# Optimization experiments

Measured on AMD Instinct MI355X. Metric: run time of the kernel, lower is better.

The kernel has to match this reference:

```python
import jax, jax.numpy as jnp
import numpy as np
from jax import lax

K = 32          # num_units (ring size / channels)
T = 100         # num_iters
FAR, NEAR = 29, 9
RING_MIN, RING_MAX, RING_BW = -0.5, 0.1, 0.5
NEAR_SUM = FAR_SUM = 0.4
H_STEP, TAU, DECAY_K = 1.0, 5.0, 1.0   # step_size, time_constant, decay_constant


def _ring_weight():
    # FeatureConnections._kernel: min-max-scaled gaussian bump, rolled per out-channel.
    X = np.linspace(0.0, 1.0, K)
    base = np.exp(-0.5 * ((X - X[K // 2]) / RING_BW) ** 2)  # pdf normalization cancels in min-max
    base = (base - base.min()) / (base.max() - base.min())
    base = base * (RING_MAX - RING_MIN) + RING_MIN
    W = np.stack([np.roll(base, K // 2 + i) for i in range(K)])  # (K_out, K_in)
    return W.astype(np.float32)


def _surround_kernel():
    # SpatialConnections._kernel: near excitation, far inhibition (opponent surround).
    inh = -FAR_SUM / (FAR ** 2 - NEAR ** 2)
    exc = NEAR_SUM / NEAR ** 2
    k = np.full((FAR, FAR), inh, dtype=np.float32)
    u = FAR // 2 - NEAR // 2
    v = FAR // 2 + NEAR // 2 + 1
    k[u:v, u:v] = exc
    return k


def setup_inputs() -> dict:
    key = jax.random.key(0)
    k1, k2, k3 = jax.random.split(key, 3)
    inbound = jax.random.normal(k1, (2, K, 64, 64), dtype=jnp.float32)
    Wf = jnp.asarray(_ring_weight())                                   # (K, K) 1x1 channel mixing
    bf = jax.random.normal(k2, (K,), dtype=jnp.float32) * 0.01        # Conv2d bias (random init in source)
    Ws = jnp.asarray(np.broadcast_to(_surround_kernel(), (K, FAR, FAR)).copy())  # diagonal (depthwise) taps
    bs = jax.random.normal(k3, (K,), dtype=jnp.float32) * 0.01
    return {"inbound": inbound, "Wf": Wf, "bf": bf, "Ws": Ws, "bs": bs}


def reference(inbound, Wf, bf, Ws, bs):
    decay = 1.0 - H_STEP * DECAY_K ** 2 / TAU   # 0.8
    gain = H_STEP / TAU                          # 0.2
    dw = Ws[:, None]                             # (K, 1, FAR, FAR) depthwise kernel (diag of full KxK conv)

    def feat(X):  # 1x1 ring-attractor channel mix
        return jnp.einsum('oi,nihw->nohw', Wf, X) + bf[None, :, None, None]

    def spat(X):  # depthwise opponent-surround conv, 'SAME' == padding (FAR-1)//2
        y = lax.conv_general_dilated(X, dw, (1, 1), 'SAME',
                                     dimension_numbers=('NCHW', 'OIHW', 'NCHW'),
                                     feature_group_count=K)
        return y + bs[None, :, None, None]

    drive = 0.5 * inbound

    def step(X, _):
        S = drive + feat(X) + spat(X)
        Xn = decay * X + gain * jax.nn.relu(S)
        return Xn, Xn

    X0 = jnp.zeros_like(inbound)
    _, Xt = lax.scan(step, X0, None, length=T)   # (T, N, K, H, W)
    return jnp.transpose(Xt, (1, 0, 2, 3, 4))    # (N, T, K, H, W)
```

## Files before the change

kernel.cpp:

```cpp
#include <hip/hip_runtime.h>

#define NN 2
#define KC 32
#define TT 100
#define HH 64
#define WW 64
#define HWSZ (HH*WW)
#define RB 4
#define RROWS 16
#define HALO 14
#define BROWS (RROWS + 2*HALO)
#define SW 65
#define NWG (NN*KC*RB)
#define FLAG_STRIDE 16

typedef float fx4 __attribute__((ext_vector_type(4)));

#define GLD8(x0,x1,x2,x3,x4,x5,x6,x7,p0,p1,p2,p3,p4,p5,p6,p7) \
  asm volatile( \
    "global_load_dwordx4 %0, %8, off sc0 sc1\n\t" \
    "global_load_dwordx4 %1, %9, off sc0 sc1\n\t" \
    "global_load_dwordx4 %2, %10, off sc0 sc1\n\t" \
    "global_load_dwordx4 %3, %11, off sc0 sc1\n\t" \
    "global_load_dwordx4 %4, %12, off sc0 sc1\n\t" \
    "global_load_dwordx4 %5, %13, off sc0 sc1\n\t" \
    "global_load_dwordx4 %6, %14, off sc0 sc1\n\t" \
    "global_load_dwordx4 %7, %15, off sc0 sc1" \
    : "=&v"(x0),"=&v"(x1),"=&v"(x2),"=&v"(x3), \
      "=&v"(x4),"=&v"(x5),"=&v"(x6),"=&v"(x7) \
    : "v"(p0),"v"(p1),"v"(p2),"v"(p3),"v"(p4),"v"(p5),"v"(p6),"v"(p7) \
    : "memory")

#define GLD3(x0,x1,x2,p0,p1,p2) \
  asm volatile( \
    "global_load_dwordx4 %0, %3, off sc0 sc1\n\t" \
    "global_load_dwordx4 %1, %4, off sc0 sc1\n\t" \
    "global_load_dwordx4 %2, %5, off sc0 sc1" \
    : "=&v"(x0),"=&v"(x1),"=&v"(x2) \
    : "v"(p0),"v"(p1),"v"(p2) : "memory")

#define VWAIT8(x0,x1,x2,x3,x4,x5,x6,x7) \
  asm volatile("s_waitcnt vmcnt(0)" \
    : "+v"(x0),"+v"(x1),"+v"(x2),"+v"(x3),"+v"(x4),"+v"(x5),"+v"(x6),"+v"(x7) \
    :: "memory")
#define VWAIT3(x0,x1,x2) \
  asm volatile("s_waitcnt vmcnt(0)" : "+v"(x0),"+v"(x1),"+v"(x2) :: "memory")

#define GST4(p, v) \
  asm volatile("global_store_dwordx4 %0, %1, off sc0 sc1" :: "v"(p), "v"(v) : "memory")

#define BAR_LDS()  asm volatile("s_waitcnt lgkmcnt(0)\n\ts_barrier" ::: "memory")
#define BAR_ONLY() asm volatile("s_barrier" ::: "memory")
#define BAR_FULL() asm volatile("s_waitcnt vmcnt(0) lgkmcnt(0)\n\ts_barrier" ::: "memory")

#define ACC(V, ch) do { const float w_ = wf[(ch)]; \
    s0 += w_*(V)[0]; s1 += w_*(V)[1]; s2 += w_*(V)[2]; s3 += w_*(V)[3]; \
    if ((ch) == c) xold = (V); } while (0)

__device__ __forceinline__ float wave_incl_scan(float v, int lane) {
  #pragma unroll
  for (int d = 1; d < 64; d <<= 1) {
    float o = __shfl_up(v, (unsigned)d, 64);
    if (lane >= d) v += o;
  }
  return v;
}

__global__ void __launch_bounds__(256, 1) ring_kernel(
    const float* __restrict__ inbound, const float* __restrict__ Wf,
    const float* __restrict__ bf, const float* __restrict__ Ws,
    const float* __restrict__ bs, float* __restrict__ out,
    unsigned* __restrict__ flags)
{
  __shared__ float I[BROWS*SW];

  const int b    = blockIdx.x;
  const int n    = b >> 7;
  const int c    = (b >> 2) & (KC-1);
  const int rb   = b & (RB-1);
  const int tid  = threadIdx.x;
  const int lane = tid & 63;
  const int wave = tid >> 6;
  const int r0   = rb * RROWS;

  const float inh = Ws[0];
  const float exc = Ws[14*29 + 14];
  const float w9  = exc - inh;

  float wf[KC];
  #pragma unroll
  for (int i = 0; i < KC; ++i) wf[i] = Wf[c*KC + i];
  const float bsum = bf[c] + bs[c];

  const int off = rb*(RROWS*WW) + tid*4;
  const float* drp = inbound + (size_t)(n*KC + c)*HWSZ + off;
  const float base0 = 0.5f*drp[0] + bsum;
  const float base1 = 0.5f*drp[1] + bsum;
  const float base2 = 0.5f*drp[2] + bsum;
  const float base3 = 0.5f*drp[3] + bsum;

  const int rl = tid >> 4;
  const int w0 = (tid & 15) * 4;
  const int br = rl + HALO;

  int  hlofs[3], hgofs[3];
  bool hval[3];
  #pragma unroll
  for (int q = 0; q < 3; ++q) {
    int id  = tid + q*256; if (id > 703) id = 703;
    int row = id >> 4;
    int c4  = (id & 15) * 4;
    int g   = r0 - HALO + row;
    hval[q]  = (g >= 0 && g < HH);
    int gc   = g < 0 ? 0 : (g > HH-1 ? HH-1 : g);
    hgofs[q] = gc*WW + c4;
    hlofs[q] = row*SW + c4;
  }

  const int ownf = ((n<<7) | (c<<2) | rb) * FLAG_STRIDE;
  int pollf = ownf;
  if (tid < 32)                  pollf = ((n<<7) | (tid<<2) | rb)    * FLAG_STRIDE;
  else if (tid == 32 && rb>0)    pollf = ((n<<7) | (c<<2) | (rb-1))  * FLAG_STRIDE;
  else if (tid == 33 && rb<RB-1) pollf = ((n<<7) | (c<<2) | (rb+1))  * FLAG_STRIDE;
  unsigned* pollp = flags + pollf;
  unsigned* ownp  = flags + ownf;

  for (int t = 0; t < TT; ++t) {
    const float* Xprev = out + (size_t)((n*TT + (t-1))*KC)*HWSZ;

    fx4 A0,A1,A2v,A3v,A4,A5,A6,A7;
    fx4 B0,B1,B2,B3,B4,B5,B6,B7;
    fx4 h0,h1,h2;

    if (t > 0) {
      if (tid < 34) {
        const unsigned tgt = (unsigned)t;
        while (__hip_atomic_load(pollp, __ATOMIC_RELAXED, __HIP_MEMORY_SCOPE_AGENT) < tgt) {
          __builtin_amdgcn_s_sleep(1);
        }
      }
      BAR_ONLY();

      const float* Xc = Xprev + (size_t)c*HWSZ;
      GLD3(h0,h1,h2, (const fx4*)(Xc+hgofs[0]),
                     (const fx4*)(Xc+hgofs[1]),
                     (const fx4*)(Xc+hgofs[2]));
      const float* Xp = Xprev + off;
      GLD8(A0,A1,A2v,A3v,A4,A5,A6,A7,
           (const fx4*)(Xp+(size_t)0*HWSZ),(const fx4*)(Xp+(size_t)1*HWSZ),
           (const fx4*)(Xp+(size_t)2*HWSZ),(const fx4*)(Xp+(size_t)3*HWSZ),
           (const fx4*)(Xp+(size_t)4*HWSZ),(const fx4*)(Xp+(size_t)5*HWSZ),
           (const fx4*)(Xp+(size_t)6*HWSZ),(const fx4*)(Xp+(size_t)7*HWSZ));
      GLD8(B0,B1,B2,B3,B4,B5,B6,B7,
           (const fx4*)(Xp+(size_t)8*HWSZ),(const fx4*)(Xp+(size_t)9*HWSZ),
           (const fx4*)(Xp+(size_t)10*HWSZ),(const fx4*)(Xp+(size_t)11*HWSZ),
           (const fx4*)(Xp+(size_t)12*HWSZ),(const fx4*)(Xp+(size_t)13*HWSZ),
           (const fx4*)(Xp+(size_t)14*HWSZ),(const fx4*)(Xp+(size_t)15*HWSZ));

      VWAIT3(h0,h1,h2);
      if (!hval[0]) h0 = fx4{0.f,0.f,0.f,0.f};
      if (!hval[1]) h1 = fx4{0.f,0.f,0.f,0.f};
      if (!hval[2]) h2 = fx4{0.f,0.f,0.f,0.f};
      I[hlofs[0]+0]=h0[0]; I[hlofs[0]+1]=h0[1]; I[hlofs[0]+2]=h0[2]; I[hlofs[0]+3]=h0[3];
      I[hlofs[1]+0]=h1[0]; I[hlofs[1]+1]=h1[1]; I[hlofs[1]+2]=h1[2]; I[hlofs[1]+3]=h1[3];
      I[hlofs[2]+0]=h2[0]; I[hlofs[2]+1]=h2[1]; I[hlofs[2]+2]=h2[2]; I[hlofs[2]+3]=h2[3];
    } else {
      for (int l = tid; l < BROWS*WW; l += 256) I[(l>>6)*SW + (l&63)] = 0.f;
    }
    BAR_LDS();

    #pragma unroll
    for (int k = 0; k < 11; ++k) {
      int row = wave*11 + k;
      float v = I[row*SW + lane];
      v = wave_incl_scan(v, lane);
      I[row*SW + lane] = v;
    }
    BAR_LDS();

    #pragma unroll
    for (int k = 0; k < 16; ++k) {
      int col = wave*16 + k;
      float v = (lane < BROWS) ? I[lane*SW + col] : 0.f;
      v = wave_incl_scan(v, lane);
      if (lane < BROWS) I[lane*SW + col] = v;
    }
    BAR_LDS();

    float s[4];
    #pragma unroll
    for (int j = 0; j < 4; ++j) {
      int w = w0 + j;
      int hi  = br + 14, lo  = br - 15;
      int whi = (w + 14 > 63) ? 63 : (w + 14);
      int wlo = w - 15;
      float b29 = I[hi*SW + whi];
      if (wlo >= 0) b29 -= I[hi*SW + wlo];
      if (lo  >= 0) { b29 -= I[lo*SW + whi]; if (wlo >= 0) b29 += I[lo*SW + wlo]; }
      int hi2  = br + 4, lo2 = br - 5;
      int whi2 = (w + 4 > 63) ? 63 : (w + 4);
      int wlo2 = w - 5;
      float b9 = I[hi2*SW + whi2];
      if (wlo2 >= 0) b9 -= I[hi2*SW + wlo2];
      b9 -= I[lo2*SW + whi2];
      if (wlo2 >= 0) b9 += I[lo2*SW + wlo2];
      s[j] = inh*b29 + w9*b9;
    }
    float s0 = base0 + s[0], s1 = base1 + s[1], s2 = base2 + s[2], s3 = base3 + s[3];

    fx4 xold = fx4{0.f,0.f,0.f,0.f};
    if (t > 0) {
      const float* Xp = Xprev + off;
      VWAIT8(A0,A1,A2v,A3v,A4,A5,A6,A7);
      VWAIT8(B0,B1,B2,B3,B4,B5,B6,B7);
      ACC(A0,0); ACC(A1,1); ACC(A2v,2); ACC(A3v,3);
      ACC(A4,4); ACC(A5,5); ACC(A6,6);  ACC(A7,7);
      GLD8(A0,A1,A2v,A3v,A4,A5,A6,A7,
           (const fx4*)(Xp+(size_t)16*HWSZ),(const fx4*)(Xp+(size_t)17*HWSZ),
           (const fx4*)(Xp+(size_t)18*HWSZ),(const fx4*)(Xp+(size_t)19*HWSZ),
           (const fx4*)(Xp+(size_t)20*HWSZ),(const fx4*)(Xp+(size_t)21*HWSZ),
           (const fx4*)(Xp+(size_t)22*HWSZ),(const fx4*)(Xp+(size_t)23*HWSZ));
      ACC(B0,8);  ACC(B1,9);  ACC(B2,10); ACC(B3,11);
      ACC(B4,12); ACC(B5,13); ACC(B6,14); ACC(B7,15);
      GLD8(B0,B1,B2,B3,B4,B5,B6,B7,
           (const fx4*)(Xp+(size_t)24*HWSZ),(const fx4*)(Xp+(size_t)25*HWSZ),
           (const fx4*)(Xp+(size_t)26*HWSZ),(const fx4*)(Xp+(size_t)27*HWSZ),
           (const fx4*)(Xp+(size_t)28*HWSZ),(const fx4*)(Xp+(size_t)29*HWSZ),
           (const fx4*)(Xp+(size_t)30*HWSZ),(const fx4*)(Xp+(size_t)31*HWSZ));
      VWAIT8(A0,A1,A2v,A3v,A4,A5,A6,A7);
      VWAIT8(B0,B1,B2,B3,B4,B5,B6,B7);
      ACC(A0,16); ACC(A1,17); ACC(A2v,18); ACC(A3v,19);
      ACC(A4,20); ACC(A5,21); ACC(A6,22);  ACC(A7,23);
      ACC(B0,24); ACC(B1,25); ACC(B2,26);  ACC(B3,27);
      ACC(B4,28); ACC(B5,29); ACC(B6,30);  ACC(B7,31);
    }

    fx4 xn;
    xn[0] = 0.8f*xold[0] + 0.2f*fmaxf(s0, 0.f);
    xn[1] = 0.8f*xold[1] + 0.2f*fmaxf(s1, 0.f);
    xn[2] = 0.8f*xold[2] + 0.2f*fmaxf(s2, 0.f);
    xn[3] = 0.8f*xold[3] + 0.2f*fmaxf(s3, 0.f);
    float* po = out + (size_t)((n*TT + t)*KC + c)*HWSZ + off;
    GST4((fx4*)po, xn);

    if (t < TT-1) {
      BAR_FULL();
      if (tid == 0) {
        __hip_atomic_store(ownp, (unsigned)(t+1), __ATOMIC_RELAXED,
                           __HIP_MEMORY_SCOPE_AGENT);
      }
    }
  }
}

extern "C" void kernel_launch(void* const* d_in, const int* in_sizes, int n_in,
                              void* d_out, int out_size, void* d_ws, size_t ws_size,
                              hipStream_t stream) {
  const float* inbound = (const float*)d_in[0];
  const float* Wf      = (const float*)d_in[1];
  const float* bf      = (const float*)d_in[2];
  const float* Ws      = (const float*)d_in[3];
  const float* bs      = (const float*)d_in[4];
  float* out = (float*)d_out;
  unsigned* flags = (unsigned*)d_ws;

  hipMemsetAsync(d_ws, 0, NWG*FLAG_STRIDE*sizeof(unsigned), stream);

  void* args[] = {(void*)&inbound, (void*)&Wf, (void*)&bf, (void*)&Ws,
                  (void*)&bs, (void*)&out, (void*)&flags};
  hipLaunchCooperativeKernel((void*)ring_kernel, dim3(NWG), dim3(256),
                             args, 0, stream);
}
```

Baseline: 1.014 ms.

## Process four channels per workgroup, reusing channel-mix loads and per-wave integral images

Each workgroup now owns a group of four channels instead of one, so the 32-channel loads of the previous state are shared across four outputs and the total grid shrinks from 256 to 64 workgroups. Each wave builds the integral image for one channel using serial per-lane row and column scans instead of shuffle-based wave scans, and the own-channel previous state is kept in registers instead of being picked out of the loaded tiles. The t=0 step skips the zeroed integral-image pass entirely. This cuts redundant global traffic and the number of workgroups that poll flags, but uses fewer CUs and adds serial LDS scan work per wave.

```diff
diff --git a/kernel.cpp b/kernel.cpp
--- a/kernel.cpp
+++ b/kernel.cpp
@@ -2,6 +2,8 @@
 
 #define NN 2
 #define KC 32
+#define G  4
+#define CG (KC/G)
 #define TT 100
 #define HH 64
 #define WW 64
@@ -11,11 +13,14 @@
 #define HALO 14
 #define BROWS (RROWS + 2*HALO)
 #define SW 65
-#define NWG (NN*KC*RB)
+#define TSZ (BROWS*SW)
+#define NWG (NN*CG*RB)
 #define FLAG_STRIDE 16
 
 typedef float fx4 __attribute__((ext_vector_type(4)));
 
+#define GLD1(x, p) \
+  asm volatile("global_load_dwordx4 %0, %1, off sc0 sc1" : "=&v"(x) : "v"(p) : "memory")
 #define GLD8(x0,x1,x2,x3,x4,x5,x6,x7,p0,p1,p2,p3,p4,p5,p6,p7) \
   asm volatile( \
     "global_load_dwordx4 %0, %8, off sc0 sc1\n\t" \
@@ -30,41 +35,20 @@
       "=&v"(x4),"=&v"(x5),"=&v"(x6),"=&v"(x7) \
     : "v"(p0),"v"(p1),"v"(p2),"v"(p3),"v"(p4),"v"(p5),"v"(p6),"v"(p7) \
     : "memory")
-
-#define GLD3(x0,x1,x2,p0,p1,p2) \
-  asm volatile( \
-    "global_load_dwordx4 %0, %3, off sc0 sc1\n\t" \
-    "global_load_dwordx4 %1, %4, off sc0 sc1\n\t" \
-    "global_load_dwordx4 %2, %5, off sc0 sc1" \
-    : "=&v"(x0),"=&v"(x1),"=&v"(x2) \
-    : "v"(p0),"v"(p1),"v"(p2) : "memory")
-
 #define VWAIT8(x0,x1,x2,x3,x4,x5,x6,x7) \
   asm volatile("s_waitcnt vmcnt(0)" \
-    : "+v"(x0),"+v"(x1),"+v"(x2),"+v"(x3),"+v"(x4),"+v"(x5),"+v"(x6),"+v"(x7) \
-    :: "memory")
-#define VWAIT3(x0,x1,x2) \
-  asm volatile("s_waitcnt vmcnt(0)" : "+v"(x0),"+v"(x1),"+v"(x2) :: "memory")
-
+    : "+v"(x0),"+v"(x1),"+v"(x2),"+v"(x3),"+v"(x4),"+v"(x5),"+v"(x6),"+v"(x7) :: "memory")
+#define VWAIT11(x0,x1,x2,x3,x4,x5,x6,x7,x8,x9,x10) \
+  asm volatile("s_waitcnt vmcnt(0)" \
+    : "+v"(x0),"+v"(x1),"+v"(x2),"+v"(x3),"+v"(x4),"+v"(x5), \
+      "+v"(x6),"+v"(x7),"+v"(x8),"+v"(x9),"+v"(x10) :: "memory")
 #define GST4(p, v) \
   asm volatile("global_store_dwordx4 %0, %1, off sc0 sc1" :: "v"(p), "v"(v) : "memory")
 
 #define BAR_LDS()  asm volatile("s_waitcnt lgkmcnt(0)\n\ts_barrier" ::: "memory")
 #define BAR_ONLY() asm volatile("s_barrier" ::: "memory")
 #define BAR_FULL() asm volatile("s_waitcnt vmcnt(0) lgkmcnt(0)\n\ts_barrier" ::: "memory")
-
-#define ACC(V, ch) do { const float w_ = wf[(ch)]; \
-    s0 += w_*(V)[0]; s1 += w_*(V)[1]; s2 += w_*(V)[2]; s3 += w_*(V)[3]; \
-    if ((ch) == c) xold = (V); } while (0)
-
-__device__ __forceinline__ float wave_incl_scan(float v, int lane) {
-  #pragma unroll
-  for (int d = 1; d < 64; d <<= 1) {
-    float o = __shfl_up(v, (unsigned)d, 64);
-    if (lane >= d) v += o;
-  }
-  return v;
-}
+#define LGKM0()    asm volatile("s_waitcnt lgkmcnt(0)" ::: "memory")
 
 __global__ void __launch_bounds__(256, 1) ring_kernel(
     const float* __restrict__ inbound, const float* __restrict__ Wf,
@@ -72,68 +56,80 @@
     const float* __restrict__ bs, float* __restrict__ out,
     unsigned* __restrict__ flags)
 {
-  __shared__ float I[BROWS*SW];
+  __shared__ float T[G*TSZ];
+  __shared__ fx4   WFS[KC];
 
   const int b    = blockIdx.x;
-  const int n    = b >> 7;
-  const int c    = (b >> 2) & (KC-1);
+  const int n    = b >> 5;
+  const int cg   = (b >> 2) & (CG-1);
   const int rb   = b & (RB-1);
   const int tid  = threadIdx.x;
   const int lane = tid & 63;
   const int wave = tid >> 6;
   const int r0   = rb * RROWS;
+  const int ch0  = cg * G;
 
   const float inh = Ws[0];
   const float exc = Ws[14*29 + 14];
   const float w9  = exc - inh;
 
-  float wf[KC];
+  if (tid < KC) {
+    fx4 wv;
+    wv[0] = Wf[(ch0+0)*KC + tid]; wv[1] = Wf[(ch0+1)*KC + tid];
+    wv[2] = Wf[(ch0+2)*KC + tid]; wv[3] = Wf[(ch0+3)*KC + tid];
+    WFS[tid] = wv;
+  }
+  BAR_LDS();
+
+  const int off = r0*WW + tid*4;
+  const int rl  = tid >> 4;
+  const int w0  = (tid & 15) * 4;
+  const int br  = rl + HALO;
+
+  fx4 base[G];
   #pragma unroll
-  for (int i = 0; i < KC; ++i) wf[i] = Wf[c*KC + i];
-  const float bsum = bf[c] + bs[c];
-
-  const int off = rb*(RROWS*WW) + tid*4;
-  const float* drp = inbound + (size_t)(n*KC + c)*HWSZ + off;
-  const float base0 = 0.5f*drp[0] + bsum;
-  const float base1 = 0.5f*drp[1] + bsum;
-  const float base2 = 0.5f*drp[2] + bsum;
-  const float base3 = 0.5f*drp[3] + bsum;
-
-  const int rl = tid >> 4;
-  const int w0 = (tid & 15) * 4;
-  const int br = rl + HALO;
-
-  int  hlofs[3], hgofs[3];
-  bool hval[3];
+  for (int j = 0; j < G; ++j) {
+    const float* dp = inbound + (size_t)(n*KC + ch0 + j)*HWSZ + off;
+    float bsum = bf[ch0+j] + bs[ch0+j];
+    base[j][0] = 0.5f*dp[0] + bsum; base[j][1] = 0.5f*dp[1] + bsum;
+    base[j][2] = 0.5f*dp[2] + bsum; base[j][3] = 0.5f*dp[3] + bsum;
+  }
+
+  int  sgofs[11], slofs[11]; bool sval[11];
   #pragma unroll
-  for (int q = 0; q < 3; ++q) {
-    int id  = tid + q*256; if (id > 703) id = 703;
+  for (int q = 0; q < 11; ++q) {
+    int id  = lane + 64*q;
     int row = id >> 4;
     int c4  = (id & 15) * 4;
     int g   = r0 - HALO + row;
-    hval[q]  = (g >= 0 && g < HH);
+    sval[q]  = (g >= 0 && g < HH);
     int gc   = g < 0 ? 0 : (g > HH-1 ? HH-1 : g);
-    hgofs[q] = gc*WW + c4;
-    hlofs[q] = row*SW + c4;
-  }
-
-  const int ownf = ((n<<7) | (c<<2) | rb) * FLAG_STRIDE;
+    sgofs[q] = gc*WW + c4;
+    slofs[q] = row*SW + c4;
+  }
+  float* Tw = T + wave*TSZ;
+
+  const int ownf = ((n<<5) | (cg<<2) | rb) * FLAG_STRIDE;
   int pollf = ownf;
-  if (tid < 32)                  pollf = ((n<<7) | (tid<<2) | rb)    * FLAG_STRIDE;
-  else if (tid == 32 && rb>0)    pollf = ((n<<7) | (c<<2) | (rb-1))  * FLAG_STRIDE;
-  else if (tid == 33 && rb<RB-1) pollf = ((n<<7) | (c<<2) | (rb+1))  * FLAG_STRIDE;
+  if (tid < CG)                  pollf = ((n<<5) | (tid<<2) | rb)    * FLAG_STRIDE;
+  else if (tid == 8 && rb>0)     pollf = ((n<<5) | (cg<<2) | (rb-1)) * FLAG_STRIDE;
+  else if (tid == 9 && rb<RB-1)  pollf = ((n<<5) | (cg<<2) | (rb+1)) * FLAG_STRIDE;
   unsigned* pollp = flags + pollf;
   unsigned* ownp  = flags + ownf;
 
+  fx4 xn[G];
+  #pragma unroll
+  for (int j = 0; j < G; ++j) xn[j] = fx4{0.f,0.f,0.f,0.f};
+
   for (int t = 0; t < TT; ++t) {
-    const float* Xprev = out + (size_t)((n*TT + (t-1))*KC)*HWSZ;
-
-    fx4 A0,A1,A2v,A3v,A4,A5,A6,A7;
-    fx4 B0,B1,B2,B3,B4,B5,B6,B7;
-    fx4 h0,h1,h2;
+    fx4 sf[G], acc[G];
+    #pragma unroll
+    for (int j = 0; j < G; ++j) { sf[j] = fx4{0,0,0,0}; acc[j] = fx4{0,0,0,0}; }
 
     if (t > 0) {
-      if (tid < 34) {
+      const float* Xprev = out + (size_t)((n*TT + (t-1))*KC)*HWSZ;
+
+      if (tid < 10) {
         const unsigned tgt = (unsigned)t;
         while (__hip_atomic_load(pollp, __ATOMIC_RELAXED, __HIP_MEMORY_SCOPE_AGENT) < tgt) {
           __builtin_amdgcn_s_sleep(1);
@@ -141,107 +137,116 @@
       }
       BAR_ONLY();
 
-      const float* Xc = Xprev + (size_t)c*HWSZ;
-      GLD3(h0,h1,h2, (const fx4*)(Xc+hgofs[0]),
-                     (const fx4*)(Xc+hgofs[1]),
-                     (const fx4*)(Xc+hgofs[2]));
+      fx4 A0,A1,A2,A3,A4,A5,A6,A7, B0,B1,B2,B3,B4,B5,B6,B7;
       const float* Xp = Xprev + off;
-      GLD8(A0,A1,A2v,A3v,A4,A5,A6,A7,
-           (const fx4*)(Xp+(size_t)0*HWSZ),(const fx4*)(Xp+(size_t)1*HWSZ),
-           (const fx4*)(Xp+(size_t)2*HWSZ),(const fx4*)(Xp+(size_t)3*HWSZ),
-           (const fx4*)(Xp+(size_t)4*HWSZ),(const fx4*)(Xp+(size_t)5*HWSZ),
-           (const fx4*)(Xp+(size_t)6*HWSZ),(const fx4*)(Xp+(size_t)7*HWSZ));
+
+      {
+        const float* Xc = Xprev + (size_t)(ch0 + wave)*HWSZ;
+        fx4 h0,h1,h2,h3,h4,h5,h6,h7,h8,h9,h10;
+        GLD1(h0,(const fx4*)(Xc+sgofs[0]));  GLD1(h1,(const fx4*)(Xc+sgofs[1]));
+        GLD1(h2,(const fx4*)(Xc+sgofs[2]));  GLD1(h3,(const fx4*)(Xc+sgofs[3]));
+        GLD1(h4,(const fx4*)(Xc+sgofs[4]));  GLD1(h5,(const fx4*)(Xc+sgofs[5]));
+        GLD1(h6,(const fx4*)(Xc+sgofs[6]));  GLD1(h7,(const fx4*)(Xc+sgofs[7]));
+        GLD1(h8,(const fx4*)(Xc+sgofs[8]));  GLD1(h9,(const fx4*)(Xc+sgofs[9]));
+        GLD1(h10,(const fx4*)(Xc+sgofs[10]));
+        GLD8(A0,A1,A2,A3,A4,A5,A6,A7,
+          (const fx4*)(Xp+(size_t)0*HWSZ),(const fx4*)(Xp+(size_t)1*HWSZ),
+          (const fx4*)(Xp+(size_t)2*HWSZ),(const fx4*)(Xp+(size_t)3*HWSZ),
+          (const fx4*)(Xp+(size_t)4*HWSZ),(const fx4*)(Xp+(size_t)5*HWSZ),
+          (const fx4*)(Xp+(size_t)6*HWSZ),(const fx4*)(Xp+(size_t)7*HWSZ));
+        GLD8(B0,B1,B2,B3,B4,B5,B6,B7,
+          (const fx4*)(Xp+(size_t)8*HWSZ),(const fx4*)(Xp+(size_t)9*HWSZ),
+          (const fx4*)(Xp+(size_t)10*HWSZ),(const fx4*)(Xp+(size_t)11*HWSZ),
+          (const fx4*)(Xp+(size_t)12*HWSZ),(const fx4*)(Xp+(size_t)13*HWSZ),
+          (const fx4*)(Xp+(size_t)14*HWSZ),(const fx4*)(Xp+(size_t)15*HWSZ));
+        VWAIT11(h0,h1,h2,h3,h4,h5,h6,h7,h8,h9,h10);
+        fx4 hh[11] = {h0,h1,h2,h3,h4,h5,h6,h7,h8,h9,h10};
+        #pragma unroll
+        for (int q = 0; q < 11; ++q) {
+          fx4 v = sval[q] ? hh[q] : fx4{0.f,0.f,0.f,0.f};
+          Tw[slofs[q]+0]=v[0]; Tw[slofs[q]+1]=v[1];
+          Tw[slofs[q]+2]=v[2]; Tw[slofs[q]+3]=v[3];
+        }
+      }
+
+      if (lane < BROWS) {
+        float* Tr = Tw + lane*SW;
+        float a = 0.f;
+        #pragma unroll 8
+        for (int cc = 0; cc < WW; ++cc) { a += Tr[cc]; Tr[cc] = a; }
+      }
+      LGKM0();
+      {
+        float* Tc = Tw + lane;
+        float a = 0.f;
+        #pragma unroll 4
+        for (int r = 0; r < BROWS; ++r) { a += Tc[r*SW]; Tc[r*SW] = a; }
+      }
+      BAR_LDS();
+
+      #pragma unroll
+      for (int j = 0; j < G; ++j) {
+        const float* Tj = T + j*TSZ;
+        #pragma unroll
+        for (int jj = 0; jj < 4; ++jj) {
+          int w = w0 + jj;
+          int hi  = br + 14, lo  = br - 15;
+          int whi = (w + 14 > 63) ? 63 : (w + 14);
+          int wlo = w - 15;
+          float b29 = Tj[hi*SW + whi];
+          if (wlo >= 0) b29 -= Tj[hi*SW + wlo];
+          if (lo  >= 0) { b29 -= Tj[lo*SW + whi]; if (wlo >= 0) b29 += Tj[lo*SW + wlo]; }
+          int hi2  = br + 4, lo2 = br - 5;
+          int whi2 = (w + 4 > 63) ? 63 : (w + 4);
+          int wlo2 = w - 5;
+          float b9 = Tj[hi2*SW + whi2];
+          if (wlo2 >= 0) b9 -= Tj[hi2*SW + wlo2];
+          b9 -= Tj[lo2*SW + whi2];
+          if (wlo2 >= 0) b9 += Tj[lo2*SW + wlo2];
+          sf[j][jj] = inh*b29 + w9*b9;
+        }
+      }
+
+      #define ACC4(V, i) do { fx4 wv = WFS[i]; \
+        acc[0] += wv[0]*(V); acc[1] += wv[1]*(V); \
+        acc[2] += wv[2]*(V); acc[3] += wv[3]*(V); } while (0)
+      VWAIT8(A0,A1,A2,A3,A4,A5,A6,A7);
+      VWAIT8(B0,B1,B2,B3,B4,B5,B6,B7);
+      ACC4(A0,0);  ACC4(A1,1);  ACC4(A2,2);  ACC4(A3,3);
+      ACC4(A4,4);  ACC4(A5,5);  ACC4(A6,6);  ACC4(A7,7);
+      GLD8(A0,A1,A2,A3,A4,A5,A6,A7,
+        (const fx4*)(Xp+(size_t)16*HWSZ),(const fx4*)(Xp+(size_t)17*HWSZ),
+        (const fx4*)(Xp+(size_t)18*HWSZ),(const fx4*)(Xp+(size_t)19*HWSZ),
+        (const fx4*)(Xp+(size_t)20*HWSZ),(const fx4*)(Xp+(size_t)21*HWSZ),
+        (const fx4*)(Xp+(size_t)22*HWSZ),(const fx4*)(Xp+(size_t)23*HWSZ));
+      ACC4(B0,8);  ACC4(B1,9);  ACC4(B2,10); ACC4(B3,11);
+      ACC4(B4,12); ACC4(B5,13); ACC4(B6,14); ACC4(B7,15);
       GLD8(B0,B1,B2,B3,B4,B5,B6,B7,
-           (const fx4*)(Xp+(size_t)8*HWSZ),(const fx4*)(Xp+(size_t)9*HWSZ),
-           (const fx4*)(Xp+(size_t)10*HWSZ),(const fx4*)(Xp+(size_t)11*HWSZ),
-           (const fx4*)(Xp+(size_t)12*HWSZ),(const fx4*)(Xp+(size_t)13*HWSZ),
-           (const fx4*)(Xp+(size_t)14*HWSZ),(const fx4*)(Xp+(size_t)15*HWSZ));
-
-      VWAIT3(h0,h1,h2);
-      if (!hval[0]) h0 = fx4{0.f,0.f,0.f,0.f};
-      if (!hval[1]) h1 = fx4{0.f,0.f,0.f,0.f};
-      if (!hval[2]) h2 = fx4{0.f,0.f,0.f,0.f};
-      I[hlofs[0]+0]=h0[0]; I[hlofs[0]+1]=h0[1]; I[hlofs[0]+2]=h0[2]; I[hlofs[0]+3]=h0[3];
-      I[hlofs[1]+0]=h1[0]; I[hlofs[1]+1]=h1[1]; I[hlofs[1]+2]=h1[2]; I[hlofs[1]+3]=h1[3];
-      I[hlofs[2]+0]=h2[0]; I[hlofs[2]+1]=h2[1]; I[hlofs[2]+2]=h2[2]; I[hlofs[2]+3]=h2[3];
-    } else {
-      for (int l = tid; l < BROWS*WW; l += 256) I[(l>>6)*SW + (l&63)] = 0.f;
+        (const fx4*)(Xp+(size_t)24*HWSZ),(const fx4*)(Xp+(size_t)25*HWSZ),
+        (const fx4*)(Xp+(size_t)26*HWSZ),(const fx4*)(Xp+(size_t)27*HWSZ),
+        (const fx4*)(Xp+(size_t)28*HWSZ),(const fx4*)(Xp+(size_t)29*HWSZ),
+        (const fx4*)(Xp+(size_t)30*HWSZ),(const fx4*)(Xp+(size_t)31*HWSZ));
+      VWAIT8(A0,A1,A2,A3,A4,A5,A6,A7);
+      VWAIT8(B0,B1,B2,B3,B4,B5,B6,B7);
+      ACC4(A0,16); ACC4(A1,17); ACC4(A2,18); ACC4(A3,19);
+      ACC4(A4,20); ACC4(A5,21); ACC4(A6,22); ACC4(A7,23);
+      ACC4(B0,24); ACC4(B1,25); ACC4(B2,26); ACC4(B3,27);
+      ACC4(B4,28); ACC4(B5,29); ACC4(B6,30); ACC4(B7,31);
+      #undef ACC4
     }
-    BAR_LDS();
-
+
+    float* ob = out + (size_t)((n*TT + t)*KC)*HWSZ + off;
     #pragma unroll
-    for (int k = 0; k < 11; ++k) {
-      int row = wave*11 + k;
-      float v = I[row*SW + lane];
-      v = wave_incl_scan(v, lane);
-      I[row*SW + lane] = v;
+    for (int j = 0; j < G; ++j) {
+      fx4 S = base[j] + sf[j] + acc[j];
+      fx4 v;
+      v[0] = 0.8f*xn[j][0] + 0.2f*fmaxf(S[0], 0.f);
+      v[1] = 0.8f*xn[j][1] + 0.2f*fmaxf(S[1], 0.f);
+      v[2] = 0.8f*xn[j][2] + 0.2f*fmaxf(S[2], 0.f);
+      v[3] = 0.8f*xn[j][3] + 0.2f*fmaxf(S[3], 0.f);
+      xn[j] = v;
+      GST4((fx4*)(ob + (size_t)(ch0+j)*HWSZ), v);
     }
-    BAR_LDS();
-
-    #pragma unroll
-    for (int k = 0; k < 16; ++k) {
-      int col = wave*16 + k;
-      float v = (lane < BROWS) ? I[lane*SW + col] : 0.f;
-      v = wave_incl_scan(v, lane);
-      if (lane < BROWS) I[lane*SW + col] = v;
-    }
-    BAR_LDS();
-
-    float s[4];
-    #pragma unroll
-    for (int j = 0; j < 4; ++j) {
-      int w = w0 + j;
-      int hi  = br + 14, lo  = br - 15;
-      int whi = (w + 14 > 63) ? 63 : (w + 14);
-      int wlo = w - 15;
-      float b29 = I[hi*SW + whi];
-      if (wlo >= 0) b29 -= I[hi*SW + wlo];
-      if (lo  >= 0) { b29 -= I[lo*SW + whi]; if (wlo >= 0) b29 += I[lo*SW + wlo]; }
-      int hi2  = br + 4, lo2 = br - 5;
-      int whi2 = (w + 4 > 63) ? 63 : (w + 4);
-      int wlo2 = w - 5;
-      float b9 = I[hi2*SW + whi2];
-      if (wlo2 >= 0) b9 -= I[hi2*SW + wlo2];
-      b9 -= I[lo2*SW + whi2];
-      if (wlo2 >= 0) b9 += I[lo2*SW + wlo2];
-      s[j] = inh*b29 + w9*b9;
-    }
-    float s0 = base0 + s[0], s1 = base1 + s[1], s2 = base2 + s[2], s3 = base3 + s[3];
-
-    fx4 xold = fx4{0.f,0.f,0.f,0.f};
-    if (t > 0) {
-      const float* Xp = Xprev + off;
-      VWAIT8(A0,A1,A2v,A3v,A4,A5,A6,A7);
-      VWAIT8(B0,B1,B2,B3,B4,B5,B6,B7);
-      ACC(A0,0); ACC(A1,1); ACC(A2v,2); ACC(A3v,3);
-      ACC(A4,4); ACC(A5,5); ACC(A6,6);  ACC(A7,7);
-      GLD8(A0,A1,A2v,A3v,A4,A5,A6,A7,
-           (const fx4*)(Xp+(size_t)16*HWSZ),(const fx4*)(Xp+(size_t)17*HWSZ),
-           (const fx4*)(Xp+(size_t)18*HWSZ),(const fx4*)(Xp+(size_t)19*HWSZ),
-           (const fx4*)(Xp+(size_t)20*HWSZ),(const fx4*)(Xp+(size_t)21*HWSZ),
-           (const fx4*)(Xp+(size_t)22*HWSZ),(const fx4*)(Xp+(size_t)23*HWSZ));
-      ACC(B0,8);  ACC(B1,9);  ACC(B2,10); ACC(B3,11);
-      ACC(B4,12); ACC(B5,13); ACC(B6,14); ACC(B7,15);
-      GLD8(B0,B1,B2,B3,B4,B5,B6,B7,
-           (const fx4*)(Xp+(size_t)24*HWSZ),(const fx4*)(Xp+(size_t)25*HWSZ),
-           (const fx4*)(Xp+(size_t)26*HWSZ),(const fx4*)(Xp+(size_t)27*HWSZ),
-           (const fx4*)(Xp+(size_t)28*HWSZ),(const fx4*)(Xp+(size_t)29*HWSZ),
-           (const fx4*)(Xp+(size_t)30*HWSZ),(const fx4*)(Xp+(size_t)31*HWSZ));
-      VWAIT8(A0,A1,A2v,A3v,A4,A5,A6,A7);
-      VWAIT8(B0,B1,B2,B3,B4,B5,B6,B7);
-      ACC(A0,16); ACC(A1,17); ACC(A2v,18); ACC(A3v,19);
-      ACC(A4,20); ACC(A5,21); ACC(A6,22);  ACC(A7,23);
-      ACC(B0,24); ACC(B1,25); ACC(B2,26);  ACC(B3,27);
-      ACC(B4,28); ACC(B5,29); ACC(B6,30);  ACC(B7,31);
-    }
-
-    fx4 xn;
-    xn[0] = 0.8f*xold[0] + 0.2f*fmaxf(s0, 0.f);
-    xn[1] = 0.8f*xold[1] + 0.2f*fmaxf(s1, 0.f);
-    xn[2] = 0.8f*xold[2] + 0.2f*fmaxf(s2, 0.f);
-    xn[3] = 0.8f*xold[3] + 0.2f*fmaxf(s3, 0.f);
-    float* po = out + (size_t)((n*TT + t)*KC + c)*HWSZ + off;
-    GST4((fx4*)po, xn);
 
     if (t < TT-1) {
       BAR_FULL();
```

New measurement: 990.4 us. -2.4%, faster.
